# Kernel optimization log

Measured on AMD Instinct MI355X. Metric: run time of the kernel, lower is better.

Reference implementation:

```python
import jax, jax.numpy as jnp
import numpy as np

EPS = 1e-5
ALPHA = 1.0

def _conv1x1(x, w, b):
    # x: [N,C,T,V], w: [O,C], b: [O] -> [N,O,T,V]
    return jnp.einsum('nctv,oc->notv', x, w) + b[None, :, None, None]

def _groupnorm1(x, gamma, beta):
    # GroupNorm(1, C): normalize over (C,T,V) per sample
    mu = jnp.mean(x, axis=(1, 2, 3), keepdims=True)
    var = jnp.var(x, axis=(1, 2, 3), keepdims=True)
    xn = (x - mu) * jax.lax.rsqrt(var + EPS)
    return xn * gamma[None, :, None, None] + beta[None, :, None, None]

def setup_inputs() -> dict:
    key = jax.random.key(0)
    ks = jax.random.split(key, 12)
    N, Cin, T, V, O, R = 128, 64, 128, 25, 64, 8
    s_in = 1.0 / np.sqrt(Cin)
    s_r = 1.0 / np.sqrt(R)
    return {
        'x':  jax.random.normal(ks[0], (N, Cin, T, V), jnp.float32),
        'A':  jax.random.normal(ks[1], (V, V), jnp.float32) * 0.1,
        'w1': jax.random.normal(ks[2], (R, Cin), jnp.float32) * s_in,
        'b1': jnp.zeros((R,), jnp.float32),
        'g1': jnp.ones((R,), jnp.float32),
        'be1': jnp.zeros((R,), jnp.float32),
        'w2': jax.random.normal(ks[3], (R, Cin), jnp.float32) * s_in,
        'b2': jnp.zeros((R,), jnp.float32),
        'g2': jnp.ones((R,), jnp.float32),
        'be2': jnp.zeros((R,), jnp.float32),
        'w3': jax.random.normal(ks[4], (O, Cin), jnp.float32) * s_in,
        'b3': jnp.zeros((O,), jnp.float32),
        'w4': jax.random.normal(ks[5], (O, R), jnp.float32) * s_r,
        'b4': jnp.zeros((O,), jnp.float32),
    }

def reference(x, A, w1, b1, g1, be1, w2, b2, g2, be2, w3, b3, w4, b4):
    # branch 1: conv1 -> GroupNorm -> temporal mean -> pairwise diff -> tanh
    x1 = _groupnorm1(_conv1x1(x, w1, b1), g1, be1).mean(axis=2)      # [N,R,V]
    y1 = jnp.tanh(x1[..., :, None] - x1[..., None, :])               # [N,R,V,V]
    # branch 2: conv2 -> GroupNorm -> temporal mean -> outer product -> tanh
    x2 = _groupnorm1(_conv1x1(x, w2, b2), g2, be2).mean(axis=2)      # [N,R,V]
    y2 = jnp.tanh(x2[..., :, None] * x2[..., None, :])               # [N,R,V,V]
    # value branch
    x3 = _conv1x1(x, w3, b3)                                          # [N,O,T,V]
    # dynamic adjacency: conv4 over rel channels
    ys = y1 + ALPHA * y2 + A[None, None]                              # [N,R,V,V]
    y_sum = jnp.einsum('nruv,or->nouv', ys, w4) + b4[None, :, None, None]
    # aggregation over vertices
    y = jnp.einsum('ncuv,nctv->nctu', y_sum, x3)                      # [N,O,T,V]
    return y
```

## Files before the change

kernel.cpp:

```cpp
#include <hip/hip_runtime.h>

#define EPSV 1e-5f
constexpr int NN = 128, CIN = 64, TT = 128, VV = 25, OO = 64, RR = 8;
constexpr int TVQ   = TT * VV;
constexpr int XSAMP = CIN * TVQ;
constexpr int YSAMP = OO * TT * VV;
constexpr int RTV   = RR * TT * VV;
constexpr int S12N  = 2 * RR * VV;
constexpr int YPAD  = 28;
constexpr int YSUMP_SAMP = OO * VV * YPAD;

__global__ __launch_bounds__(256) void kZero(float* __restrict__ p, int n)
{
    int i = blockIdx.x * 256 + threadIdx.x;
    if (i < n) p[i] = 0.f;
}

__global__ __launch_bounds__(256) void kA(const float* __restrict__ x,
    const float* __restrict__ w1, const float* __restrict__ b1,
    const float* __restrict__ w2, const float* __restrict__ b2,
    float* __restrict__ s12g, float* __restrict__ ssqg)
{
    __shared__ float wt1[CIN * RR], wt2[CIN * RR];
    __shared__ float s1l[RR * VV], s2l[RR * VV];
    __shared__ float redA[4], redB[4];
    const int tid = threadIdx.x;
    const int tc  = blockIdx.x;
    const int n   = blockIdx.y;

    for (int e = tid; e < CIN * RR; e += 256) {
        int r = e >> 6, c = e & 63;
        wt1[c * RR + r] = w1[e];
        wt2[c * RR + r] = w2[e];
    }
    for (int e = tid; e < 2 * RR * VV; e += 256) {
        if (e < RR * VV) s1l[e] = 0.f; else s2l[e - RR * VV] = 0.f;
    }
    __syncthreads();

    float acc1[4][RR], acc2[4][RR];
    #pragma unroll
    for (int j = 0; j < 4; ++j)
        #pragma unroll
        for (int r = 0; r < RR; ++r) { acc1[j][r] = 0.f; acc2[j][r] = 0.f; }

    const bool active = (tid < 200);
    const int p0 = tid * 4;
    const float* xb = x + (size_t)n * XSAMP + tc * 800 + p0;
    if (active) {
        #pragma unroll 4
        for (int c = 0; c < CIN; ++c) {
            float4 xv  = *(const float4*)(xb + c * TVQ);
            float4 wa1 = *(const float4*)(&wt1[c * RR]);
            float4 wb1 = *(const float4*)(&wt1[c * RR + 4]);
            float4 wa2 = *(const float4*)(&wt2[c * RR]);
            float4 wb2 = *(const float4*)(&wt2[c * RR + 4]);
            float xj[4]  = {xv.x, xv.y, xv.z, xv.w};
            float w1v[8] = {wa1.x, wa1.y, wa1.z, wa1.w, wb1.x, wb1.y, wb1.z, wb1.w};
            float w2v[8] = {wa2.x, wa2.y, wa2.z, wa2.w, wb2.x, wb2.y, wb2.z, wb2.w};
            #pragma unroll
            for (int j = 0; j < 4; ++j)
                #pragma unroll
                for (int r = 0; r < RR; ++r) {
                    acc1[j][r] += w1v[r] * xj[j];
                    acc2[j][r] += w2v[r] * xj[j];
                }
        }
    }

    float b1r[RR], b2r[RR];
    #pragma unroll
    for (int r = 0; r < RR; ++r) { b1r[r] = b1[r]; b2r[r] = b2[r]; }

    float ssq1 = 0.f, ssq2 = 0.f;
    if (active) {
        #pragma unroll
        for (int j = 0; j < 4; ++j) {
            int v = (p0 + j) % VV;
            #pragma unroll
            for (int r = 0; r < RR; ++r) {
                float c1 = acc1[j][r] + b1r[r]; ssq1 += c1 * c1;
                float c2 = acc2[j][r] + b2r[r]; ssq2 += c2 * c2;
                atomicAdd(&s1l[r * VV + v], acc1[j][r]);
                atomicAdd(&s2l[r * VV + v], acc2[j][r]);
            }
        }
    }
    #pragma unroll
    for (int off = 32; off > 0; off >>= 1) {
        ssq1 += __shfl_down(ssq1, off);
        ssq2 += __shfl_down(ssq2, off);
    }
    __syncthreads();
    for (int e = tid; e < S12N; e += 256) {
        float pv = (e < RR * VV) ? s1l[e] : s2l[e - RR * VV];
        atomicAdd(&s12g[n * S12N + e], pv);
    }
    if ((tid & 63) == 0) { redA[tid >> 6] = ssq1; redB[tid >> 6] = ssq2; }
    __syncthreads();
    if (tid == 0) {
        atomicAdd(&ssqg[n * 2 + 0], redA[0] + redA[1] + redA[2] + redA[3]);
        atomicAdd(&ssqg[n * 2 + 1], redB[0] + redB[1] + redB[2] + redB[3]);
    }
}

__device__ __forceinline__ float tanh_fast(float v)
{
    float e = __expf(2.f * v);
    return 1.f - 2.f / (e + 1.f);
}

__global__ __launch_bounds__(512) void kB(
    const float* __restrict__ s12g, const float* __restrict__ ssqg,
    const float* __restrict__ b1, const float* __restrict__ g1, const float* __restrict__ be1,
    const float* __restrict__ b2, const float* __restrict__ g2, const float* __restrict__ be2,
    const float* __restrict__ Amat, const float* __restrict__ w4, const float* __restrict__ b4,
    float* __restrict__ ysump)
{
    __shared__ float x1g[RR * VV], x2g[RR * VV];
    __shared__ float w4l[OO * RR];
    __shared__ float stats[2];
    __shared__ float mss[4];
    const int tid = threadIdx.x;
    const int n   = blockIdx.x;

    if (tid < 2) stats[tid] = 0.f;
    for (int e = tid; e < OO * RR; e += 512) w4l[e] = w4[e];
    __syncthreads();

    float sv = 0.f;
    if (tid < S12N) {
        sv = s12g[n * S12N + tid];
        atomicAdd(&stats[tid / (RR * VV)], sv);
    }
    __syncthreads();
    if (tid == 0) {
        float sb1 = 0.f, sb2 = 0.f;
        for (int r = 0; r < RR; ++r) { sb1 += b1[r]; sb2 += b2[r]; }
        float mu1 = (stats[0] + (float)(TT * VV) * sb1) / (float)RTV;
        float mu2 = (stats[1] + (float)(TT * VV) * sb2) / (float)RTV;
        float var1 = ssqg[n * 2 + 0] / (float)RTV - mu1 * mu1;
        float var2 = ssqg[n * 2 + 1] / (float)RTV - mu2 * mu2;
        mss[0] = mu1; mss[1] = rsqrtf(var1 + EPSV);
        mss[2] = mu2; mss[3] = rsqrtf(var2 + EPSV);
    }
    __syncthreads();
    if (tid < S12N) {
        int br = tid / (RR * VV);
        int i  = tid % (RR * VV);
        int r  = i / VV;
        float mu = mss[br * 2], rs = mss[br * 2 + 1];
        float mean_t = sv / (float)TT + (br ? b2[r] : b1[r]);
        float g  = br ? g2[r]  : g1[r];
        float be = br ? be2[r] : be1[r];
        float val = g * (mean_t - mu) * rs + be;
        if (br == 0) x1g[i] = val; else x2g[i] = val;
    }
    __syncthreads();

    float* yn = ysump + (size_t)n * YSUMP_SAMP;
    for (int p = tid; p < VV * VV; p += 512) {
        int u = p / VV, v = p % VV;
        float Av = Amat[p];
        float ys[RR];
        #pragma unroll
        for (int r = 0; r < RR; ++r) {
            float d = x1g[r * VV + u] - x1g[r * VV + v];
            float m = x2g[r * VV + u] * x2g[r * VV + v];
            ys[r] = tanh_fast(d) + tanh_fast(m) + Av;
        }
        for (int o = 0; o < OO; ++o) {
            float a = b4[o];
            #pragma unroll
            for (int r = 0; r < RR; ++r) a += w4l[o * RR + r] * ys[r];
            yn[(o * VV + u) * YPAD + v] = a;
        }
    }
    for (int q = tid; q < OO * VV * 3; q += 512) {
        int o = q / (VV * 3), rem = q % (VV * 3);
        int u = rem / 3, v = VV + rem % 3;
        yn[(o * VV + u) * YPAD + v] = 0.f;
    }
}

__global__ __launch_bounds__(512, 4) void kC(
    const float* __restrict__ x, const float* __restrict__ w3,
    const float* __restrict__ b3, const float* __restrict__ ysump,
    float* __restrict__ y)
{
    __shared__ float xl[CIN * 8 * 28];
    __shared__ float ysl[OO * 29];
    const int tid = threadIdx.x;
    const int o   = tid & 63;
    const int th  = tid >> 6;
    const int tc  = blockIdx.x;
    const int n   = blockIdx.y;
    const int t0  = tc * 8;

    const float* xn = x + (size_t)n * XSAMP + t0 * VV;
    for (int e = tid; e < CIN * 8 * VV; e += 512) {
        int c = e / 200, rem = e % 200;
        int t = rem / VV, v = rem % VV;
        xl[c * 224 + t * 28 + v] = xn[c * TVQ + rem];
    }
    __syncthreads();

    float acc[VV];
    #pragma unroll
    for (int i = 0; i < VV; ++i) acc[i] = 0.f;

    #pragma unroll 1
    for (int half = 0; half < 2; ++half) {
        float w3r[32];
        #pragma unroll
        for (int q = 0; q < 8; ++q) {
            float4 wv = *(const float4*)(w3 + o * CIN + half * 32 + q * 4);
            w3r[q*4+0] = wv.x; w3r[q*4+1] = wv.y; w3r[q*4+2] = wv.z; w3r[q*4+3] = wv.w;
        }
        #pragma unroll
        for (int ci = 0; ci < 32; ++ci) {
            const float* p = &xl[(half * 32 + ci) * 224 + th * 28];
            const float w = w3r[ci];
            float4 a0 = *(const float4*)(p + 0);
            float4 a1 = *(const float4*)(p + 4);
            float4 a2 = *(const float4*)(p + 8);
            float4 a3 = *(const float4*)(p + 12);
            float4 a4 = *(const float4*)(p + 16);
            float4 a5 = *(const float4*)(p + 20);
            float  a6 = p[24];
            acc[0]  += w*a0.x; acc[1]  += w*a0.y; acc[2]  += w*a0.z; acc[3]  += w*a0.w;
            acc[4]  += w*a1.x; acc[5]  += w*a1.y; acc[6]  += w*a1.z; acc[7]  += w*a1.w;
            acc[8]  += w*a2.x; acc[9]  += w*a2.y; acc[10] += w*a2.z; acc[11] += w*a2.w;
            acc[12] += w*a3.x; acc[13] += w*a3.y; acc[14] += w*a3.z; acc[15] += w*a3.w;
            acc[16] += w*a4.x; acc[17] += w*a4.y; acc[18] += w*a4.z; acc[19] += w*a4.w;
            acc[20] += w*a5.x; acc[21] += w*a5.y; acc[22] += w*a5.z; acc[23] += w*a5.w;
            acc[24] += w*a6;
        }
    }
    const float bias = b3[o];
    #pragma unroll
    for (int i = 0; i < VV; ++i) acc[i] += bias;

    const float* ysn = ysump + (size_t)n * YSUMP_SAMP;
    for (int u = 0; u < VV; ++u) {
        __syncthreads();
        for (int e = tid; e < OO * VV; e += 512) {
            int oo = e / VV, vv = e % VV;
            ysl[oo * 29 + vv] = ysn[(oo * VV + u) * YPAD + vv];
        }
        __syncthreads();
        const float* yr = &ysl[o * 29];
        float s = 0.f;
        #pragma unroll
        for (int v = 0; v < VV; ++v) s += yr[v] * acc[v];
        xl[o * 200 + th * VV + u] = s;
    }
    __syncthreads();
    float* yb = y + (size_t)n * YSAMP + t0 * VV;
    for (int idx = tid; idx < (OO * 8 * VV) / 4; idx += 512) {
        int oo = idx / 50, rem = idx % 50;
        *(float4*)(yb + oo * TVQ + rem * 4) = *(const float4*)(&xl[idx * 4]);
    }
}

extern "C" void kernel_launch(void* const* d_in, const int* in_sizes, int n_in,
                              void* d_out, int out_size, void* d_ws, size_t ws_size,
                              hipStream_t stream)
{
    const float* x   = (const float*)d_in[0];
    const float* Am  = (const float*)d_in[1];
    const float* w1  = (const float*)d_in[2];
    const float* b1  = (const float*)d_in[3];
    const float* g1  = (const float*)d_in[4];
    const float* be1 = (const float*)d_in[5];
    const float* w2  = (const float*)d_in[6];
    const float* b2  = (const float*)d_in[7];
    const float* g2  = (const float*)d_in[8];
    const float* be2 = (const float*)d_in[9];
    const float* w3  = (const float*)d_in[10];
    const float* b3  = (const float*)d_in[11];
    const float* w4  = (const float*)d_in[12];
    const float* b4  = (const float*)d_in[13];
    float* y  = (float*)d_out;
    float* ws = (float*)d_ws;
    float* s12g  = ws;
    float* ssqg  = ws + NN * S12N;
    float* ysump = ws + NN * S12N + NN * 2;

    const int nz = NN * S12N + NN * 2;
    hipLaunchKernelGGL(kZero, dim3((nz + 255) / 256), dim3(256), 0, stream, ws, nz);
    hipLaunchKernelGGL(kA, dim3(4, NN), dim3(256), 0, stream,
                       x, w1, b1, w2, b2, s12g, ssqg);
    hipLaunchKernelGGL(kB, dim3(NN), dim3(512), 0, stream,
                       s12g, ssqg, b1, g1, be1, b2, g2, be2, Am, w4, b4, ysump);
    hipLaunchKernelGGL(kC, dim3(16, NN), dim3(512), 0, stream,
                       x, w3, b3, ysump, y);
}
```

Before: 514.5 us.

## Retile aggregation kernel with two time rows per thread and chunked ysum loads

kC now runs 256 threads, each computing two time rows, so every w3 weight register is reused twice. The adjacency matrix is staged in chunks of 8 vertices instead of one vertex per barrier, which cuts the number of __syncthreads from 25 to 4, and outputs are written directly to global memory. kB is split across 5 blocks per sample to raise parallelism, and one barrier is removed from kA. In exchange, kC uses more registers per thread and writes outputs as strided scalar stores rather than float4.

Measured after the change: 644.0 us. 1.25x slower.

```diff
diff --git a/kernel.cpp b/kernel.cpp
--- a/kernel.cpp
+++ b/kernel.cpp
@@ -91,13 +91,12 @@
         ssq1 += __shfl_down(ssq1, off);
         ssq2 += __shfl_down(ssq2, off);
     }
+    if ((tid & 63) == 0) { redA[tid >> 6] = ssq1; redB[tid >> 6] = ssq2; }
     __syncthreads();
     for (int e = tid; e < S12N; e += 256) {
         float pv = (e < RR * VV) ? s1l[e] : s2l[e - RR * VV];
         atomicAdd(&s12g[n * S12N + e], pv);
     }
-    if ((tid & 63) == 0) { redA[tid >> 6] = ssq1; redB[tid >> 6] = ssq2; }
-    __syncthreads();
     if (tid == 0) {
         atomicAdd(&ssqg[n * 2 + 0], redA[0] + redA[1] + redA[2] + redA[3]);
         atomicAdd(&ssqg[n * 2 + 1], redB[0] + redB[1] + redB[2] + redB[3]);
@@ -119,13 +118,16 @@
 {
     __shared__ float x1g[RR * VV], x2g[RR * VV];
     __shared__ float w4l[OO * RR];
+    __shared__ float b4l[OO];
     __shared__ float stats[2];
     __shared__ float mss[4];
     const int tid = threadIdx.x;
-    const int n   = blockIdx.x;
+    const int bx  = blockIdx.x;
+    const int n   = blockIdx.y;
 
     if (tid < 2) stats[tid] = 0.f;
-    for (int e = tid; e < OO * RR; e += 512) w4l[e] = w4[e];
+    if (tid < OO * RR) w4l[tid] = w4[tid];
+    if (tid < OO) b4l[tid] = b4[tid];
     __syncthreads();
 
     float sv = 0.f;
@@ -159,7 +161,8 @@
     __syncthreads();
 
     float* yn = ysump + (size_t)n * YSUMP_SAMP;
-    for (int p = tid; p < VV * VV; p += 512) {
+    const int pend = (bx + 1) * 125;
+    for (int p = bx * 125 + tid; p < pend; p += 512) {
         int u = p / VV, v = p % VV;
         float Av = Amat[p];
         float ys[RR];
@@ -170,26 +173,27 @@
             ys[r] = tanh_fast(d) + tanh_fast(m) + Av;
         }
         for (int o = 0; o < OO; ++o) {
-            float a = b4[o];
+            float a = b4l[o];
             #pragma unroll
             for (int r = 0; r < RR; ++r) a += w4l[o * RR + r] * ys[r];
             yn[(o * VV + u) * YPAD + v] = a;
         }
     }
-    for (int q = tid; q < OO * VV * 3; q += 512) {
-        int o = q / (VV * 3), rem = q % (VV * 3);
-        int u = rem / 3, v = VV + rem % 3;
-        yn[(o * VV + u) * YPAD + v] = 0.f;
-    }
-}
-
-__global__ __launch_bounds__(512, 4) void kC(
+    if (bx == 0) {
+        for (int q = tid; q < OO * VV * 3; q += 512) {
+            int o = q / (VV * 3), rem = q % (VV * 3);
+            int u = rem / 3, v = VV + rem % 3;
+            yn[(o * VV + u) * YPAD + v] = 0.f;
+        }
+    }
+}
+
+__global__ __launch_bounds__(256) void kC(
     const float* __restrict__ x, const float* __restrict__ w3,
     const float* __restrict__ b3, const float* __restrict__ ysump,
     float* __restrict__ y)
 {
-    __shared__ float xl[CIN * 8 * 28];
-    __shared__ float ysl[OO * 29];
+    __shared__ float lds[14400];
     const int tid = threadIdx.x;
     const int o   = tid & 63;
     const int th  = tid >> 6;
@@ -198,16 +202,21 @@
     const int t0  = tc * 8;
 
     const float* xn = x + (size_t)n * XSAMP + t0 * VV;
-    for (int e = tid; e < CIN * 8 * VV; e += 512) {
-        int c = e / 200, rem = e % 200;
-        int t = rem / VV, v = rem % VV;
-        xl[c * 224 + t * 28 + v] = xn[c * TVQ + rem];
-    }
-    __syncthreads();
-
-    float acc[VV];
-    #pragma unroll
-    for (int i = 0; i < VV; ++i) acc[i] = 0.f;
+    for (int e4 = tid; e4 < CIN * 50; e4 += 256) {
+        int c = e4 / 50, r4 = (e4 % 50) * 4;
+        float4 tmp = *(const float4*)(xn + c * TVQ + r4);
+        float tv[4] = {tmp.x, tmp.y, tmp.z, tmp.w};
+        #pragma unroll
+        for (int j = 0; j < 4; ++j) {
+            int rem = r4 + j;
+            lds[c * 224 + (rem / VV) * 28 + (rem % VV)] = tv[j];
+        }
+    }
+    __syncthreads();
+
+    float acc0[VV], acc1[VV];
+    #pragma unroll
+    for (int i = 0; i < VV; ++i) { acc0[i] = 0.f; acc1[i] = 0.f; }
 
     #pragma unroll 1
     for (int half = 0; half < 2; ++half) {
@@ -219,47 +228,64 @@
         }
         #pragma unroll
         for (int ci = 0; ci < 32; ++ci) {
-            const float* p = &xl[(half * 32 + ci) * 224 + th * 28];
             const float w = w3r[ci];
-            float4 a0 = *(const float4*)(p + 0);
-            float4 a1 = *(const float4*)(p + 4);
-            float4 a2 = *(const float4*)(p + 8);
-            float4 a3 = *(const float4*)(p + 12);
-            float4 a4 = *(const float4*)(p + 16);
-            float4 a5 = *(const float4*)(p + 20);
-            float  a6 = p[24];
-            acc[0]  += w*a0.x; acc[1]  += w*a0.y; acc[2]  += w*a0.z; acc[3]  += w*a0.w;
-            acc[4]  += w*a1.x; acc[5]  += w*a1.y; acc[6]  += w*a1.z; acc[7]  += w*a1.w;
-            acc[8]  += w*a2.x; acc[9]  += w*a2.y; acc[10] += w*a2.z; acc[11] += w*a2.w;
-            acc[12] += w*a3.x; acc[13] += w*a3.y; acc[14] += w*a3.z; acc[15] += w*a3.w;
-            acc[16] += w*a4.x; acc[17] += w*a4.y; acc[18] += w*a4.z; acc[19] += w*a4.w;
-            acc[20] += w*a5.x; acc[21] += w*a5.y; acc[22] += w*a5.z; acc[23] += w*a5.w;
-            acc[24] += w*a6;
+            const float* p = &lds[(half * 32 + ci) * 224 + (2 * th) * 28];
+            #pragma unroll
+            for (int row = 0; row < 2; ++row) {
+                float* a = row ? acc1 : acc0;
+                const float* pr = p + row * 28;
+                float4 a0 = *(const float4*)(pr + 0);
+                float4 a1 = *(const float4*)(pr + 4);
+                float4 a2 = *(const float4*)(pr + 8);
+                float4 a3 = *(const float4*)(pr + 12);
+                float4 a4 = *(const float4*)(pr + 16);
+                float4 a5 = *(const float4*)(pr + 20);
+                float  a6 = pr[24];
+                a[0]  += w*a0.x; a[1]  += w*a0.y; a[2]  += w*a0.z; a[3]  += w*a0.w;
+                a[4]  += w*a1.x; a[5]  += w*a1.y; a[6]  += w*a1.z; a[7]  += w*a1.w;
+                a[8]  += w*a2.x; a[9]  += w*a2.y; a[10] += w*a2.z; a[11] += w*a2.w;
+                a[12] += w*a3.x; a[13] += w*a3.y; a[14] += w*a3.z; a[15] += w*a3.w;
+                a[16] += w*a4.x; a[17] += w*a4.y; a[18] += w*a4.z; a[19] += w*a4.w;
+                a[20] += w*a5.x; a[21] += w*a5.y; a[22] += w*a5.z; a[23] += w*a5.w;
+                a[24] += w*a6;
+            }
         }
     }
     const float bias = b3[o];
     #pragma unroll
-    for (int i = 0; i < VV; ++i) acc[i] += bias;
+    for (int i = 0; i < VV; ++i) { acc0[i] += bias; acc1[i] += bias; }
 
     const float* ysn = ysump + (size_t)n * YSUMP_SAMP;
-    for (int u = 0; u < VV; ++u) {
+    float* yb = y + (size_t)n * YSAMP + (size_t)o * TVQ + t0 * VV;
+    #pragma unroll 1
+    for (int chunk = 0; chunk < 4; ++chunk) {
+        const int u0 = chunk * 8;
+        const int cs = (u0 + 8 <= VV) ? 8 : (VV - u0);
         __syncthreads();
-        for (int e = tid; e < OO * VV; e += 512) {
-            int oo = e / VV, vv = e % VV;
-            ysl[oo * 29 + vv] = ysn[(oo * VV + u) * YPAD + vv];
+        for (int e4 = tid; e4 < 64 * cs * 7; e4 += 256) {
+            int oo = e4 / (cs * 7), k4 = (e4 % (cs * 7)) * 4;
+            float4 tmp = *(const float4*)(ysn + oo * 700 + u0 * 28 + k4);
+            float* dst = &lds[oo * 225 + k4];
+            dst[0] = tmp.x; dst[1] = tmp.y; dst[2] = tmp.z; dst[3] = tmp.w;
         }
         __syncthreads();
-        const float* yr = &ysl[o * 29];
-        float s = 0.f;
-        #pragma unroll
-        for (int v = 0; v < VV; ++v) s += yr[v] * acc[v];
-        xl[o * 200 + th * VV + u] = s;
-    }
-    __syncthreads();
-    float* yb = y + (size_t)n * YSAMP + t0 * VV;
-    for (int idx = tid; idx < (OO * 8 * VV) / 4; idx += 512) {
-        int oo = idx / 50, rem = idx % 50;
-        *(float4*)(yb + oo * TVQ + rem * 4) = *(const float4*)(&xl[idx * 4]);
+        #pragma unroll 1
+        for (int uu = 0; uu < cs; ++uu) {
+            const float* yr = &lds[o * 225 + uu * 28];
+            float s0a = 0.f, s0b = 0.f, s1a = 0.f, s1b = 0.f;
+            #pragma unroll
+            for (int v = 0; v < 24; v += 2) {
+                float ya = yr[v], yb2 = yr[v + 1];
+                s0a += ya * acc0[v];     s0b += yb2 * acc0[v + 1];
+                s1a += ya * acc1[v];     s1b += yb2 * acc1[v + 1];
+            }
+            float y24 = yr[24];
+            s0a += y24 * acc0[24];
+            s1a += y24 * acc1[24];
+            const int u = u0 + uu;
+            yb[(2 * th) * VV + u]     = s0a + s0b;
+            yb[(2 * th + 1) * VV + u] = s1a + s1b;
+        }
     }
 }
 
@@ -291,8 +317,8 @@
     hipLaunchKernelGGL(kZero, dim3((nz + 255) / 256), dim3(256), 0, stream, ws, nz);
     hipLaunchKernelGGL(kA, dim3(4, NN), dim3(256), 0, stream,
                        x, w1, b1, w2, b2, s12g, ssqg);
-    hipLaunchKernelGGL(kB, dim3(NN), dim3(512), 0, stream,
+    hipLaunchKernelGGL(kB, dim3(5, NN), dim3(512), 0, stream,
                        s12g, ssqg, b1, g1, be1, b2, g2, be2, Am, w4, b4, ysump);
-    hipLaunchKernelGGL(kC, dim3(16, NN), dim3(512), 0, stream,
+    hipLaunchKernelGGL(kC, dim3(16, NN), dim3(256), 0, stream,
                        x, w3, b3, ysump, y);
 }
```
